# Kernel optimization log

Measured on AMD Instinct MI355X. Metric: run time of the kernel, lower is better.

## Reference

```python
import jax, jax.numpy as jnp
import numpy as np

DIM = 256
NUM_HEADS = 8
HEAD_DIM = DIM // NUM_HEADS
SCALE = HEAD_DIM ** -0.5
KSIZE = 5


def setup_inputs() -> dict:
    key = jax.random.key(0)
    ks = jax.random.split(key, 6)
    B, C, H, W = 8, DIM, 32, 32
    x = jax.random.normal(ks[0], (B, C, H, W), dtype=jnp.float32)
    qkv_w = jax.random.normal(ks[1], (3 * C, C), dtype=jnp.float32) * 0.02  # 1x1 conv, no bias
    proj_w = jax.random.normal(ks[2], (C, C), dtype=jnp.float32) * 0.02    # 1x1 conv
    proj_b = jax.random.normal(ks[3], (C,), dtype=jnp.float32) * 0.02
    lepe_w = jax.random.normal(ks[4], (C, 1, KSIZE, KSIZE), dtype=jnp.float32) * 0.02  # depthwise
    lepe_b = jax.random.normal(ks[5], (C,), dtype=jnp.float32) * 0.02
    return {"x": x, "qkv_w": qkv_w, "proj_w": proj_w, "proj_b": proj_b,
            "lepe_w": lepe_w, "lepe_b": lepe_b}


def _forward(x, qkv_w, proj_w, proj_b, lepe_w, lepe_b):
    B, C, H, W = x.shape
    N = H * W
    # 1x1 conv qkv: [B,3C,H,W]
    qkv = jnp.einsum('bchw,oc->bohw', x, qkv_w)
    q, k, v = jnp.split(qkv, 3, axis=1)
    # reshape to [B, heads, head_dim, N]
    qh = q.reshape(B, NUM_HEADS, HEAD_DIM, N)
    kh = k.reshape(B, NUM_HEADS, HEAD_DIM, N)
    vh = v.reshape(B, NUM_HEADS, HEAD_DIM, N)
    # attn = (q^T k) * scale, softmax over keys -> [B, heads, N, N]
    attn = jnp.einsum('bhdn,bhdm->bhnm', qh, kh)
    attn = jax.nn.softmax(attn * SCALE, axis=-1)
    # out = attn @ v^T -> [B, heads, N, head_dim] -> [B, C, H, W]
    out = jnp.einsum('bhnm,bhdm->bhdn', attn, vh).reshape(B, C, H, W)
    # LePE: depthwise conv on v (image layout) + residual add
    lepe = jax.lax.conv_general_dilated(
        v, lepe_w, window_strides=(1, 1),
        padding=[(KSIZE // 2, KSIZE // 2)] * 2,
        dimension_numbers=('NCHW', 'OIHW', 'NCHW'),
        feature_group_count=C) + lepe_b[None, :, None, None]
    out = out + lepe
    # 1x1 proj
    out = jnp.einsum('bchw,oc->bohw', out, proj_w) + proj_b[None, :, None, None]
    return out


def reference(x, qkv_w, proj_w, proj_b, lepe_w, lepe_b):
    return _forward(x, qkv_w, proj_w, proj_b, lepe_w, lepe_b)
```

## Files before the change

kernel.cpp:

```cpp
#include <hip/hip_runtime.h>

#define NB 8
#define NC 256
#define NN 1024

typedef unsigned short u16;
typedef unsigned int u32;
typedef __attribute__((ext_vector_type(8))) short short8;
typedef __attribute__((ext_vector_type(4))) float f32x4;

__device__ __forceinline__ u16 f2b(float f){ union{float ff;u32 i;}v; v.ff=f; u32 r=v.i+0x7FFFu+((v.i>>16)&1u); return (u16)(r>>16); }
__device__ __forceinline__ float b2f(u16 p){ union{u32 i;float f;}v; v.i=((u32)p)<<16; return v.f; }
__device__ __forceinline__ float pklo(u32 p){ union{u32 i;float f;}v; v.i=p<<16; return v.f; }
__device__ __forceinline__ float pkhi(u32 p){ union{u32 i;float f;}v; v.i=p&0xFFFF0000u; return v.f; }

#define QSC 0.25503486f

union FR { uint4 u; short8 s; };

__global__ void __launch_bounds__(256) k_cast(const float* __restrict__ qkvw,
                                              const float* __restrict__ projw,
                                              const float* __restrict__ x,
                                              u16* __restrict__ wb,
                                              u16* __restrict__ xt){
  __shared__ u16 lt[64][136];
  const int tid = threadIdx.x;
  if (blockIdx.x < 256){
    const int idx = blockIdx.x*256 + tid;
    const float* src = (idx < 49152) ? (qkvw + (size_t)idx*4)
                                     : (projw + (size_t)(idx-49152)*4);
    float4 a = *(const float4*)src;
    uint2 o;
    o.x = (u32)f2b(a.x) | ((u32)f2b(a.y)<<16);
    o.y = (u32)f2b(a.z) | ((u32)f2b(a.w)<<16);
    *(uint2*)(wb + (size_t)idx*4) = o;
    return;
  }
  const int bx = blockIdx.x - 256;
  const int n0 = (bx & 15)*64, c0 = ((bx>>4)&1)*128, b = bx>>5;
  #pragma unroll
  for (int cc = 0; cc < 4; cc++){
    const int c = c0 + cc*32 + (tid>>3);
    const int ns = (tid&7)*8;
    const float* src = x + ((size_t)(b*NC + c))*NN + n0 + ns;
    float4 a = *(const float4*)src;
    float4 d = *(const float4*)(src+4);
    const int cl = c - c0;
    lt[ns+0][cl] = f2b(a.x); lt[ns+1][cl] = f2b(a.y);
    lt[ns+2][cl] = f2b(a.z); lt[ns+3][cl] = f2b(a.w);
    lt[ns+4][cl] = f2b(d.x); lt[ns+5][cl] = f2b(d.y);
    lt[ns+6][cl] = f2b(d.z); lt[ns+7][cl] = f2b(d.w);
  }
  __syncthreads();
  #pragma unroll
  for (int p = 0; p < 4; p++){
    const int flat = p*256 + tid;
    const int row = flat >> 4, seg = flat & 15;
    uint4 d = *(uint4*)&lt[row][seg*8];
    *(uint4*)(xt + ((size_t)(b*NN + n0 + row))*NC + c0 + seg*8) = d;
  }
}

__global__ void __launch_bounds__(256) k_qkv(const u16* __restrict__ wqb,
                                             const u16* __restrict__ xt,
                                             u16* __restrict__ qt,
                                             u16* __restrict__ kt,
                                             u16* __restrict__ v){
  const int ot = blockIdx.x, nt = blockIdx.y, b = blockIdx.z;
  const int o0 = ot*32;
  const int tid = threadIdx.x, wv = tid>>6, lane = tid&63;
  const int l15 = lane&15, quad = lane>>4;
  const int n0w = nt*256 + wv*64;
  __shared__ u16 swq[32][264];
  __shared__ u16 s2[4][64][40];
  #pragma unroll
  for (int i = 0; i < 4; i++){
    const int flat = i*256 + tid;
    const int row = flat >> 5, col = flat & 31;
    *(uint4*)&swq[row][col*8] = *(const uint4*)(wqb + (size_t)(o0+row)*NC + col*8);
  }
  __syncthreads();
  f32x4 acc[2][4];
  #pragma unroll
  for (int mt = 0; mt < 2; mt++)
    #pragma unroll
    for (int nt2 = 0; nt2 < 4; nt2++) acc[mt][nt2] = (f32x4){0.f,0.f,0.f,0.f};
  const u16* xb = xt + ((size_t)(b*NN + n0w))*NC;
  for (int k0 = 0; k0 < 256; k0 += 32){
    FR af[2], bf[4];
    af[0].u = *(uint4*)&swq[l15][k0 + quad*8];
    af[1].u = *(uint4*)&swq[16+l15][k0 + quad*8];
    #pragma unroll
    for (int nt2 = 0; nt2 < 4; nt2++)
      bf[nt2].u = *(const uint4*)(xb + (size_t)(nt2*16+l15)*NC + k0 + quad*8);
    #pragma unroll
    for (int mt = 0; mt < 2; mt++)
      #pragma unroll
      for (int nt2 = 0; nt2 < 4; nt2++)
        acc[mt][nt2] = __builtin_amdgcn_mfma_f32_16x16x32_bf16(af[mt].s, bf[nt2].s, acc[mt][nt2], 0,0,0);
  }
  if (ot < 16){
    const float sc = (ot < 8) ? QSC : 1.0f;
    u16* dstbase = (ot < 8) ? qt : kt;
    const int h = (ot < 8) ? ot : ot-8;
    #pragma unroll
    for (int mt = 0; mt < 2; mt++)
      #pragma unroll
      for (int nt2 = 0; nt2 < 4; nt2++){
        uint2 w;
        w.x = (u32)f2b(acc[mt][nt2][0]*sc) | ((u32)f2b(acc[mt][nt2][1]*sc)<<16);
        w.y = (u32)f2b(acc[mt][nt2][2]*sc) | ((u32)f2b(acc[mt][nt2][3]*sc)<<16);
        *(uint2*)&s2[wv][nt2*16+l15][mt*16+quad*4] = w;
      }
    __syncthreads();
    u16* db = dstbase + ((size_t)(b*8+h)*NN + n0w)*32;
    #pragma unroll
    for (int p = 0; p < 4; p++){
      const int n_loc = p*16 + (lane>>2), seg = lane&3;
      uint4 d = *(uint4*)&s2[wv][n_loc][seg*8];
      *(uint4*)(db + (size_t)n_loc*32 + seg*8) = d;
    }
  } else {
    const int c0 = o0 - 512;
    #pragma unroll
    for (int mt = 0; mt < 2; mt++)
      #pragma unroll
      for (int nt2 = 0; nt2 < 4; nt2++)
        #pragma unroll
        for (int r = 0; r < 4; r++)
          v[(size_t)(b*NC + c0 + mt*16 + quad*4 + r)*NN + n0w + nt2*16 + l15] = f2b(acc[mt][nt2][r]);
  }
}

__global__ void __launch_bounds__(256) k_attn(const u16* __restrict__ qt,
                                              const u16* __restrict__ kt,
                                              const u16* __restrict__ v,
                                              const float* __restrict__ lw,
                                              const float* __restrict__ lb,
                                              u16* __restrict__ tt){
  const int h = blockIdx.y, b = blockIdx.z;
  const int tid = threadIdx.x;
  const int wv = tid >> 6, lane = tid & 63;
  const int l15 = lane & 15, quad = lane >> 4;
  const int bh = b*8 + h;
  const int q0 = (blockIdx.x*4 + wv)*32;

  __shared__ u16 pb[4][2][16][40];
  __shared__ u16 vstage[8][32][38];
  __shared__ u16 s_out[4][32][36];
  u16* pbA = &pb[wv][0][0][0];
  u16* pbB = &pb[wv][1][0][0];

  {
    const int rr = tid >> 5, lc2 = tid & 31;
    const int yy = blockIdx.x*4 - 2 + rr;
    u32* dst32 = (u32*)&vstage[rr][lc2][0];
    if (yy < 0 || yy > 31){
      #pragma unroll
      for (int j = 0; j < 19; j++) dst32[j] = 0;
    } else {
      const u16* src = v + ((size_t)(b*NC + h*32 + lc2))*NN + yy*32;
      uint4 a = *(const uint4*)src;
      uint4 b4 = *(const uint4*)(src+8);
      uint4 c4 = *(const uint4*)(src+16);
      uint4 d4 = *(const uint4*)(src+24);
      dst32[0] = 0;
      dst32[1]=a.x;  dst32[2]=a.y;  dst32[3]=a.z;  dst32[4]=a.w;
      dst32[5]=b4.x; dst32[6]=b4.y; dst32[7]=b4.z; dst32[8]=b4.w;
      dst32[9]=c4.x; dst32[10]=c4.y; dst32[11]=c4.z; dst32[12]=c4.w;
      dst32[13]=d4.x; dst32[14]=d4.y; dst32[15]=d4.z; dst32[16]=d4.w;
      dst32[17]=0; dst32[18]=0;
    }
  }
  __syncthreads();

  const u16* qtb = qt + (size_t)bh*NN*32;
  const u16* ktb = kt + (size_t)bh*NN*32;
  const u16* vbp = v + (size_t)(b*256 + h*32)*NN;

  FR qa, qb_;
  qa.u  = *(const uint4*)(qtb + (size_t)(q0      + l15)*32 + quad*8);
  qb_.u = *(const uint4*)(qtb + (size_t)(q0 + 16 + l15)*32 + quad*8);

  f32x4 z = {0.f,0.f,0.f,0.f};
  f32x4 oA0 = z, oA1 = z, oB0 = z, oB1 = z;
  float denA[4] = {0.f,0.f,0.f,0.f}, denB[4] = {0.f,0.f,0.f,0.f};

  for (int m0 = 0; m0 < NN; m0 += 32){
    FR kf0, kf1, vf0, vf1;
    kf0.u = *(const uint4*)(ktb + (size_t)(m0      + l15)*32 + quad*8);
    kf1.u = *(const uint4*)(ktb + (size_t)(m0 + 16 + l15)*32 + quad*8);
    vf0.u = *(const uint4*)(vbp + (size_t)(l15     )*NN + m0 + quad*8);
    vf1.u = *(const uint4*)(vbp + (size_t)(16 + l15)*NN + m0 + quad*8);

    f32x4 sA0 = __builtin_amdgcn_mfma_f32_16x16x32_bf16(qa.s,  kf0.s, z, 0,0,0);
    f32x4 sA1 = __builtin_amdgcn_mfma_f32_16x16x32_bf16(qa.s,  kf1.s, z, 0,0,0);
    f32x4 sB0 = __builtin_amdgcn_mfma_f32_16x16x32_bf16(qb_.s, kf0.s, z, 0,0,0);
    f32x4 sB1 = __builtin_amdgcn_mfma_f32_16x16x32_bf16(qb_.s, kf1.s, z, 0,0,0);

    #pragma unroll
    for (int r = 0; r < 4; r++){
      float pA0 = __builtin_amdgcn_exp2f(sA0[r]);
      float pA1 = __builtin_amdgcn_exp2f(sA1[r]);
      float pB0 = __builtin_amdgcn_exp2f(sB0[r]);
      float pB1 = __builtin_amdgcn_exp2f(sB1[r]);
      denA[r] += pA0 + pA1;
      denB[r] += pB0 + pB1;
      const int row = (quad*4 + r)*40;
      pbA[row + l15]      = (u16)(__float_as_uint(pA0)>>16);
      pbA[row + 16 + l15] = (u16)(__float_as_uint(pA1)>>16);
      pbB[row + l15]      = (u16)(__float_as_uint(pB0)>>16);
      pbB[row + 16 + l15] = (u16)(__float_as_uint(pB1)>>16);
    }
    FR pfA, pfB;
    pfA.u = *(const uint4*)(pbA + l15*40 + quad*8);
    pfB.u = *(const uint4*)(pbB + l15*40 + quad*8);

    oA0 = __builtin_amdgcn_mfma_f32_16x16x32_bf16(pfA.s, vf0.s, oA0, 0,0,0);
    oA1 = __builtin_amdgcn_mfma_f32_16x16x32_bf16(pfA.s, vf1.s, oA1, 0,0,0);
    oB0 = __builtin_amdgcn_mfma_f32_16x16x32_bf16(pfB.s, vf0.s, oB0, 0,0,0);
    oB1 = __builtin_amdgcn_mfma_f32_16x16x32_bf16(pfB.s, vf1.s, oB1, 0,0,0);
  }
  #pragma unroll
  for (int r = 0; r < 4; r++){
    #pragma unroll
    for (int m = 1; m < 16; m <<= 1){
      denA[r] += __shfl_xor(denA[r], m);
      denB[r] += __shfl_xor(denB[r], m);
    }
  }
  {
    u16* so = &s_out[wv][0][0];
    #pragma unroll
    for (int r = 0; r < 4; r++){
      const int q = quad*4 + r;
      const float iA = 1.f/denA[r], iB = 1.f/denB[r];
      so[q*36 + l15]           = f2b(oA0[r]*iA);
      so[q*36 + 16 + l15]      = f2b(oA1[r]*iA);
      so[(q+16)*36 + l15]      = f2b(oB0[r]*iB);
      so[(q+16)*36 + 16 + l15] = f2b(oB1[r]*iB);
    }
  }
  {
    const int lc = lane & 31, qh = lane >> 5;
    float lep[16];
    const float lbias = lb[h*32 + lc];
    #pragma unroll
    for (int i = 0; i < 16; i++) lep[i] = lbias;
    const float* lwc = lw + (size_t)(h*32 + lc)*25;
    #pragma unroll
    for (int ky = 0; ky < 5; ky++){
      const u32* vr = (const u32*)&vstage[wv + ky][lc][0];
      float vv[20];
      #pragma unroll
      for (int jj = 0; jj < 10; jj++){
        u32 pk = vr[qh*8 + jj];
        vv[2*jj]   = pklo(pk);
        vv[2*jj+1] = pkhi(pk);
      }
      const float w0 = lwc[ky*5+0], w1 = lwc[ky*5+1], w2 = lwc[ky*5+2],
                  w3 = lwc[ky*5+3], w4 = lwc[ky*5+4];
      #pragma unroll
      for (int i = 0; i < 16; i++)
        lep[i] += w0*vv[i] + w1*vv[i+1] + w2*vv[i+2] + w3*vv[i+3] + w4*vv[i+4];
    }
    u16* tb = tt + ((size_t)(b*NN + q0))*NC + h*32;
    const u16* so = &s_out[wv][0][0];
    #pragma unroll
    for (int i = 0; i < 16; i++){
      const int q = qh*16 + i;
      tb[(size_t)q*NC + lc] = f2b(b2f(so[q*36 + lc]) + lep[i]);
    }
  }
}

__global__ void __launch_bounds__(256) k_proj(const u16* __restrict__ wpb,
                                              const u16* __restrict__ tt,
                                              const float* __restrict__ pbias,
                                              float* __restrict__ out){
  const int ot = blockIdx.x, nt = blockIdx.y, b = blockIdx.z;
  const int o0 = ot*32;
  const int tid = threadIdx.x, wv = tid>>6, lane = tid&63;
  const int l15 = lane&15, quad = lane>>4;
  const int n0w = nt*256 + wv*64;
  __shared__ u16 swp[32][264];
  #pragma unroll
  for (int i = 0; i < 4; i++){
    const int flat = i*256 + tid;
    const int row = flat >> 5, col = flat & 31;
    *(uint4*)&swp[row][col*8] = *(const uint4*)(wpb + (size_t)(o0+row)*NC + col*8);
  }
  __syncthreads();
  f32x4 acc[2][4];
  #pragma unroll
  for (int mt = 0; mt < 2; mt++)
    #pragma unroll
    for (int nt2 = 0; nt2 < 4; nt2++) acc[mt][nt2] = (f32x4){0.f,0.f,0.f,0.f};
  const u16* tb = tt + ((size_t)(b*NN + n0w))*NC;
  for (int k0 = 0; k0 < 256; k0 += 32){
    FR af[2], bf[4];
    af[0].u = *(uint4*)&swp[l15][k0 + quad*8];
    af[1].u = *(uint4*)&swp[16+l15][k0 + quad*8];
    #pragma unroll
    for (int nt2 = 0; nt2 < 4; nt2++)
      bf[nt2].u = *(const uint4*)(tb + (size_t)(nt2*16+l15)*NC + k0 + quad*8);
    #pragma unroll
    for (int mt = 0; mt < 2; mt++)
      #pragma unroll
      for (int nt2 = 0; nt2 < 4; nt2++)
        acc[mt][nt2] = __builtin_amdgcn_mfma_f32_16x16x32_bf16(af[mt].s, bf[nt2].s, acc[mt][nt2], 0,0,0);
  }
  float bv[2][4];
  #pragma unroll
  for (int mt = 0; mt < 2; mt++)
    #pragma unroll
    for (int r = 0; r < 4; r++) bv[mt][r] = pbias[o0 + mt*16 + quad*4 + r];
  #pragma unroll
  for (int mt = 0; mt < 2; mt++)
    #pragma unroll
    for (int nt2 = 0; nt2 < 4; nt2++)
      #pragma unroll
      for (int r = 0; r < 4; r++)
        out[(size_t)(b*NC + o0 + mt*16 + quad*4 + r)*NN + n0w + nt2*16 + l15] = acc[mt][nt2][r] + bv[mt][r];
}

extern "C" void kernel_launch(void* const* d_in, const int* in_sizes, int n_in,
                              void* d_out, int out_size, void* d_ws, size_t ws_size,
                              hipStream_t stream){
  const float* x      = (const float*)d_in[0];
  const float* qkv_w  = (const float*)d_in[1];
  const float* proj_w = (const float*)d_in[2];
  const float* proj_b = (const float*)d_in[3];
  const float* lepe_w = (const float*)d_in[4];
  const float* lepe_b = (const float*)d_in[5];
  float* out = (float*)d_out;

  if (ws_size < (size_t)21495808) return;
  u16* wqb = (u16*)d_ws;
  u16* wpb = wqb + 196608;
  u16* xt  = wpb + 65536;
  u16* qt  = xt + 2097152;
  u16* kt  = qt + 2097152;
  u16* v   = kt + 2097152;
  u16* tt  = v  + 2097152;

  k_cast<<<dim3(512),     256, 0, stream>>>(qkv_w, proj_w, x, wqb, xt);
  k_qkv <<<dim3(24, 4, 8),256, 0, stream>>>(wqb, xt, qt, kt, v);
  k_attn<<<dim3(8, 8, 8), 256, 0, stream>>>(qt, kt, v, lepe_w, lepe_b, tt);
  k_proj<<<dim3(8, 4, 8), 256, 0, stream>>>(wpb, tt, proj_b, out);
}
```

Measured before the change: 121.8 us.

## Software-pipeline attention loop, fuse weight casts into GEMMs, remap grids

```diff
diff --git a/kernel.cpp b/kernel.cpp
--- a/kernel.cpp
+++ b/kernel.cpp
@@ -18,26 +18,11 @@
 
 union FR { uint4 u; short8 s; };
 
-__global__ void __launch_bounds__(256) k_cast(const float* __restrict__ qkvw,
-                                              const float* __restrict__ projw,
-                                              const float* __restrict__ x,
-                                              u16* __restrict__ wb,
+__global__ void __launch_bounds__(256) k_cast(const float* __restrict__ x,
                                               u16* __restrict__ xt){
+  const int n0 = blockIdx.x*64, c0 = blockIdx.y*128, b = blockIdx.z;
+  const int tid = threadIdx.x;
   __shared__ u16 lt[64][136];
-  const int tid = threadIdx.x;
-  if (blockIdx.x < 256){
-    const int idx = blockIdx.x*256 + tid;
-    const float* src = (idx < 49152) ? (qkvw + (size_t)idx*4)
-                                     : (projw + (size_t)(idx-49152)*4);
-    float4 a = *(const float4*)src;
-    uint2 o;
-    o.x = (u32)f2b(a.x) | ((u32)f2b(a.y)<<16);
-    o.y = (u32)f2b(a.z) | ((u32)f2b(a.w)<<16);
-    *(uint2*)(wb + (size_t)idx*4) = o;
-    return;
-  }
-  const int bx = blockIdx.x - 256;
-  const int n0 = (bx & 15)*64, c0 = ((bx>>4)&1)*128, b = bx>>5;
   #pragma unroll
   for (int cc = 0; cc < 4; cc++){
     const int c = c0 + cc*32 + (tid>>3);
@@ -61,12 +46,13 @@
   }
 }
 
-__global__ void __launch_bounds__(256) k_qkv(const u16* __restrict__ wqb,
+__global__ void __launch_bounds__(256) k_qkv(const float* __restrict__ wq,
                                              const u16* __restrict__ xt,
                                              u16* __restrict__ qt,
                                              u16* __restrict__ kt,
                                              u16* __restrict__ v){
-  const int ot = blockIdx.x, nt = blockIdx.y, b = blockIdx.z;
+  const int ot = blockIdx.x >> 5, nb = blockIdx.x & 31;
+  const int nt = nb >> 3, b = nb & 7;
   const int o0 = ot*32;
   const int tid = threadIdx.x, wv = tid>>6, lane = tid&63;
   const int l15 = lane&15, quad = lane>>4;
@@ -74,10 +60,14 @@
   __shared__ u16 swq[32][264];
   __shared__ u16 s2[4][64][40];
   #pragma unroll
-  for (int i = 0; i < 4; i++){
+  for (int i = 0; i < 8; i++){
     const int flat = i*256 + tid;
-    const int row = flat >> 5, col = flat & 31;
-    *(uint4*)&swq[row][col*8] = *(const uint4*)(wqb + (size_t)(o0+row)*NC + col*8);
+    const int row = flat >> 6, c4 = flat & 63;
+    float4 a = *(const float4*)(wq + (size_t)(o0+row)*NC + c4*4);
+    uint2 p;
+    p.x = (u32)f2b(a.x) | ((u32)f2b(a.y)<<16);
+    p.y = (u32)f2b(a.z) | ((u32)f2b(a.w)<<16);
+    *(uint2*)&swq[row][c4*4] = p;
   }
   __syncthreads();
   f32x4 acc[2][4];
@@ -138,22 +128,20 @@
                                               const float* __restrict__ lw,
                                               const float* __restrict__ lb,
                                               u16* __restrict__ tt){
-  const int h = blockIdx.y, b = blockIdx.z;
+  const int cq = blockIdx.x >> 6, bh = blockIdx.x & 63;
+  const int b = bh >> 3, h = bh & 7;
   const int tid = threadIdx.x;
   const int wv = tid >> 6, lane = tid & 63;
   const int l15 = lane & 15, quad = lane >> 4;
-  const int bh = b*8 + h;
-  const int q0 = (blockIdx.x*4 + wv)*32;
-
-  __shared__ u16 pb[4][2][16][40];
+  const int q0 = (cq*4 + wv)*32;
+
+  __shared__ u16 pb[4][2][2][16][40];
   __shared__ u16 vstage[8][32][38];
   __shared__ u16 s_out[4][32][36];
-  u16* pbA = &pb[wv][0][0][0];
-  u16* pbB = &pb[wv][1][0][0];
 
   {
     const int rr = tid >> 5, lc2 = tid & 31;
-    const int yy = blockIdx.x*4 - 2 + rr;
+    const int yy = cq*4 - 2 + rr;
     u32* dst32 = (u32*)&vstage[rr][lc2][0];
     if (yy < 0 || yy > 31){
       #pragma unroll
@@ -186,18 +174,19 @@
   f32x4 oA0 = z, oA1 = z, oB0 = z, oB1 = z;
   float denA[4] = {0.f,0.f,0.f,0.f}, denB[4] = {0.f,0.f,0.f,0.f};
 
-  for (int m0 = 0; m0 < NN; m0 += 32){
-    FR kf0, kf1, vf0, vf1;
-    kf0.u = *(const uint4*)(ktb + (size_t)(m0      + l15)*32 + quad*8);
-    kf1.u = *(const uint4*)(ktb + (size_t)(m0 + 16 + l15)*32 + quad*8);
-    vf0.u = *(const uint4*)(vbp + (size_t)(l15     )*NN + m0 + quad*8);
-    vf1.u = *(const uint4*)(vbp + (size_t)(16 + l15)*NN + m0 + quad*8);
-
-    f32x4 sA0 = __builtin_amdgcn_mfma_f32_16x16x32_bf16(qa.s,  kf0.s, z, 0,0,0);
-    f32x4 sA1 = __builtin_amdgcn_mfma_f32_16x16x32_bf16(qa.s,  kf1.s, z, 0,0,0);
-    f32x4 sB0 = __builtin_amdgcn_mfma_f32_16x16x32_bf16(qb_.s, kf0.s, z, 0,0,0);
-    f32x4 sB1 = __builtin_amdgcn_mfma_f32_16x16x32_bf16(qb_.s, kf1.s, z, 0,0,0);
-
+  FR kc0, kc1, vc0, vc1;
+  kc0.u = *(const uint4*)(ktb + (size_t)(l15     )*32 + quad*8);
+  kc1.u = *(const uint4*)(ktb + (size_t)(16 + l15)*32 + quad*8);
+  vc0.u = *(const uint4*)(vbp + (size_t)(l15     )*NN + quad*8);
+  vc1.u = *(const uint4*)(vbp + (size_t)(16 + l15)*NN + quad*8);
+
+  {
+    f32x4 sA0 = __builtin_amdgcn_mfma_f32_16x16x32_bf16(qa.s,  kc0.s, z, 0,0,0);
+    f32x4 sA1 = __builtin_amdgcn_mfma_f32_16x16x32_bf16(qa.s,  kc1.s, z, 0,0,0);
+    f32x4 sB0 = __builtin_amdgcn_mfma_f32_16x16x32_bf16(qb_.s, kc0.s, z, 0,0,0);
+    f32x4 sB1 = __builtin_amdgcn_mfma_f32_16x16x32_bf16(qb_.s, kc1.s, z, 0,0,0);
+    u16* pA = &pb[wv][0][0][0][0];
+    u16* pB = &pb[wv][0][1][0][0];
     #pragma unroll
     for (int r = 0; r < 4; r++){
       float pA0 = __builtin_amdgcn_exp2f(sA0[r]);
@@ -207,20 +196,66 @@
       denA[r] += pA0 + pA1;
       denB[r] += pB0 + pB1;
       const int row = (quad*4 + r)*40;
-      pbA[row + l15]      = (u16)(__float_as_uint(pA0)>>16);
-      pbA[row + 16 + l15] = (u16)(__float_as_uint(pA1)>>16);
-      pbB[row + l15]      = (u16)(__float_as_uint(pB0)>>16);
-      pbB[row + 16 + l15] = (u16)(__float_as_uint(pB1)>>16);
-    }
+      pA[row + l15]      = (u16)(__float_as_uint(pA0)>>16);
+      pA[row + 16 + l15] = (u16)(__float_as_uint(pA1)>>16);
+      pB[row + l15]      = (u16)(__float_as_uint(pB0)>>16);
+      pB[row + 16 + l15] = (u16)(__float_as_uint(pB1)>>16);
+    }
+  }
+
+  for (int it = 1; it < 32; it++){
+    const int m0 = it*32;
+    FR kn0, kn1, vn0, vn1;
+    kn0.u = *(const uint4*)(ktb + (size_t)(m0      + l15)*32 + quad*8);
+    kn1.u = *(const uint4*)(ktb + (size_t)(m0 + 16 + l15)*32 + quad*8);
+    vn0.u = *(const uint4*)(vbp + (size_t)(l15     )*NN + m0 + quad*8);
+    vn1.u = *(const uint4*)(vbp + (size_t)(16 + l15)*NN + m0 + quad*8);
+
+    {
+      const u16* pbr = &pb[wv][(it-1)&1][0][0][0];
+      FR pfA, pfB;
+      pfA.u = *(const uint4*)(pbr + l15*40 + quad*8);
+      pfB.u = *(const uint4*)(pbr + 640 + l15*40 + quad*8);
+      oA0 = __builtin_amdgcn_mfma_f32_16x16x32_bf16(pfA.s, vc0.s, oA0, 0,0,0);
+      oA1 = __builtin_amdgcn_mfma_f32_16x16x32_bf16(pfA.s, vc1.s, oA1, 0,0,0);
+      oB0 = __builtin_amdgcn_mfma_f32_16x16x32_bf16(pfB.s, vc0.s, oB0, 0,0,0);
+      oB1 = __builtin_amdgcn_mfma_f32_16x16x32_bf16(pfB.s, vc1.s, oB1, 0,0,0);
+    }
+    {
+      f32x4 sA0 = __builtin_amdgcn_mfma_f32_16x16x32_bf16(qa.s,  kn0.s, z, 0,0,0);
+      f32x4 sA1 = __builtin_amdgcn_mfma_f32_16x16x32_bf16(qa.s,  kn1.s, z, 0,0,0);
+      f32x4 sB0 = __builtin_amdgcn_mfma_f32_16x16x32_bf16(qb_.s, kn0.s, z, 0,0,0);
+      f32x4 sB1 = __builtin_amdgcn_mfma_f32_16x16x32_bf16(qb_.s, kn1.s, z, 0,0,0);
+      u16* pA = &pb[wv][it&1][0][0][0];
+      u16* pB = &pb[wv][it&1][1][0][0];
+      #pragma unroll
+      for (int r = 0; r < 4; r++){
+        float pA0 = __builtin_amdgcn_exp2f(sA0[r]);
+        float pA1 = __builtin_amdgcn_exp2f(sA1[r]);
+        float pB0 = __builtin_amdgcn_exp2f(sB0[r]);
+        float pB1 = __builtin_amdgcn_exp2f(sB1[r]);
+        denA[r] += pA0 + pA1;
+        denB[r] += pB0 + pB1;
+        const int row = (quad*4 + r)*40;
+        pA[row + l15]      = (u16)(__float_as_uint(pA0)>>16);
+        pA[row + 16 + l15] = (u16)(__float_as_uint(pA1)>>16);
+        pB[row + l15]      = (u16)(__float_as_uint(pB0)>>16);
+        pB[row + 16 + l15] = (u16)(__float_as_uint(pB1)>>16);
+      }
+    }
+    kc0 = kn0; kc1 = kn1; vc0 = vn0; vc1 = vn1;
+  }
+  {
+    const u16* pbr = &pb[wv][1][0][0][0];
     FR pfA, pfB;
-    pfA.u = *(const uint4*)(pbA + l15*40 + quad*8);
-    pfB.u = *(const uint4*)(pbB + l15*40 + quad*8);
-
-    oA0 = __builtin_amdgcn_mfma_f32_16x16x32_bf16(pfA.s, vf0.s, oA0, 0,0,0);
-    oA1 = __builtin_amdgcn_mfma_f32_16x16x32_bf16(pfA.s, vf1.s, oA1, 0,0,0);
-    oB0 = __builtin_amdgcn_mfma_f32_16x16x32_bf16(pfB.s, vf0.s, oB0, 0,0,0);
-    oB1 = __builtin_amdgcn_mfma_f32_16x16x32_bf16(pfB.s, vf1.s, oB1, 0,0,0);
-  }
+    pfA.u = *(const uint4*)(pbr + l15*40 + quad*8);
+    pfB.u = *(const uint4*)(pbr + 640 + l15*40 + quad*8);
+    oA0 = __builtin_amdgcn_mfma_f32_16x16x32_bf16(pfA.s, vc0.s, oA0, 0,0,0);
+    oA1 = __builtin_amdgcn_mfma_f32_16x16x32_bf16(pfA.s, vc1.s, oA1, 0,0,0);
+    oB0 = __builtin_amdgcn_mfma_f32_16x16x32_bf16(pfB.s, vc0.s, oB0, 0,0,0);
+    oB1 = __builtin_amdgcn_mfma_f32_16x16x32_bf16(pfB.s, vc1.s, oB1, 0,0,0);
+  }
+
   #pragma unroll
   for (int r = 0; r < 4; r++){
     #pragma unroll
@@ -274,41 +309,45 @@
   }
 }
 
-__global__ void __launch_bounds__(256) k_proj(const u16* __restrict__ wpb,
+__global__ void __launch_bounds__(256) k_proj(const float* __restrict__ wp,
                                               const u16* __restrict__ tt,
                                               const float* __restrict__ pbias,
                                               float* __restrict__ out){
-  const int ot = blockIdx.x, nt = blockIdx.y, b = blockIdx.z;
+  const int ot = blockIdx.x >> 6, rest = blockIdx.x & 63;
+  const int nt = rest >> 3, b = rest & 7;
   const int o0 = ot*32;
   const int tid = threadIdx.x, wv = tid>>6, lane = tid&63;
   const int l15 = lane&15, quad = lane>>4;
-  const int n0w = nt*256 + wv*64;
+  const int n0w = nt*128 + wv*32;
   __shared__ u16 swp[32][264];
   #pragma unroll
-  for (int i = 0; i < 4; i++){
+  for (int i = 0; i < 8; i++){
     const int flat = i*256 + tid;
-    const int row = flat >> 5, col = flat & 31;
-    *(uint4*)&swp[row][col*8] = *(const uint4*)(wpb + (size_t)(o0+row)*NC + col*8);
+    const int row = flat >> 6, c4 = flat & 63;
+    float4 a = *(const float4*)(wp + (size_t)(o0+row)*NC + c4*4);
+    uint2 p;
+    p.x = (u32)f2b(a.x) | ((u32)f2b(a.y)<<16);
+    p.y = (u32)f2b(a.z) | ((u32)f2b(a.w)<<16);
+    *(uint2*)&swp[row][c4*4] = p;
   }
   __syncthreads();
-  f32x4 acc[2][4];
+  f32x4 acc[2][2];
   #pragma unroll
   for (int mt = 0; mt < 2; mt++)
     #pragma unroll
-    for (int nt2 = 0; nt2 < 4; nt2++) acc[mt][nt2] = (f32x4){0.f,0.f,0.f,0.f};
+    for (int n2 = 0; n2 < 2; n2++) acc[mt][n2] = (f32x4){0.f,0.f,0.f,0.f};
   const u16* tb = tt + ((size_t)(b*NN + n0w))*NC;
   for (int k0 = 0; k0 < 256; k0 += 32){
-    FR af[2], bf[4];
+    FR af[2], bf[2];
     af[0].u = *(uint4*)&swp[l15][k0 + quad*8];
     af[1].u = *(uint4*)&swp[16+l15][k0 + quad*8];
-    #pragma unroll
-    for (int nt2 = 0; nt2 < 4; nt2++)
-      bf[nt2].u = *(const uint4*)(tb + (size_t)(nt2*16+l15)*NC + k0 + quad*8);
+    bf[0].u = *(const uint4*)(tb + (size_t)(l15     )*NC + k0 + quad*8);
+    bf[1].u = *(const uint4*)(tb + (size_t)(16 + l15)*NC + k0 + quad*8);
     #pragma unroll
     for (int mt = 0; mt < 2; mt++)
       #pragma unroll
-      for (int nt2 = 0; nt2 < 4; nt2++)
-        acc[mt][nt2] = __builtin_amdgcn_mfma_f32_16x16x32_bf16(af[mt].s, bf[nt2].s, acc[mt][nt2], 0,0,0);
+      for (int n2 = 0; n2 < 2; n2++)
+        acc[mt][n2] = __builtin_amdgcn_mfma_f32_16x16x32_bf16(af[mt].s, bf[n2].s, acc[mt][n2], 0,0,0);
   }
   float bv[2][4];
   #pragma unroll
@@ -318,10 +357,10 @@
   #pragma unroll
   for (int mt = 0; mt < 2; mt++)
     #pragma unroll
-    for (int nt2 = 0; nt2 < 4; nt2++)
+    for (int n2 = 0; n2 < 2; n2++)
       #pragma unroll
       for (int r = 0; r < 4; r++)
-        out[(size_t)(b*NC + o0 + mt*16 + quad*4 + r)*NN + n0w + nt2*16 + l15] = acc[mt][nt2][r] + bv[mt][r];
+        out[(size_t)(b*NC + o0 + mt*16 + quad*4 + r)*NN + n0w + n2*16 + l15] = acc[mt][n2][r] + bv[mt][r];
 }
 
 extern "C" void kernel_launch(void* const* d_in, const int* in_sizes, int n_in,
@@ -335,17 +374,15 @@
   const float* lepe_b = (const float*)d_in[5];
   float* out = (float*)d_out;
 
-  if (ws_size < (size_t)21495808) return;
-  u16* wqb = (u16*)d_ws;
-  u16* wpb = wqb + 196608;
-  u16* xt  = wpb + 65536;
-  u16* qt  = xt + 2097152;
-  u16* kt  = qt + 2097152;
-  u16* v   = kt + 2097152;
-  u16* tt  = v  + 2097152;
-
-  k_cast<<<dim3(512),     256, 0, stream>>>(qkv_w, proj_w, x, wqb, xt);
-  k_qkv <<<dim3(24, 4, 8),256, 0, stream>>>(wqb, xt, qt, kt, v);
-  k_attn<<<dim3(8, 8, 8), 256, 0, stream>>>(qt, kt, v, lepe_w, lepe_b, tt);
-  k_proj<<<dim3(8, 4, 8), 256, 0, stream>>>(wpb, tt, proj_b, out);
-}
+  if (ws_size < (size_t)20*1024*1024) return;
+  u16* xt = (u16*)d_ws;
+  u16* qt = xt + 2097152;
+  u16* kt = qt + 2097152;
+  u16* v  = kt + 2097152;
+  u16* tt = v  + 2097152;
+
+  k_cast<<<dim3(16, 2, 8), 256, 0, stream>>>(x, xt);
+  k_qkv <<<dim3(768),      256, 0, stream>>>(qkv_w, xt, qt, kt, v);
+  k_attn<<<dim3(512),      256, 0, stream>>>(qt, kt, v, lepe_w, lepe_b, tt);
+  k_proj<<<dim3(512),      256, 0, stream>>>(proj_w, tt, proj_b, out);
+}
```

Result: no change. 123.0 us (+0.9%).
